# Kernel optimization log

Hardware: AMD Instinct MI355X
Metric: run time of the kernel (lower is better)

The kernel has to match this reference:

```python
import jax, jax.numpy as jnp
import numpy as np

B, C, W, H = 8192, 512, 14, 4
D = C // H  # head dim = 128


def setup_inputs() -> dict:
    key = jax.random.key(0)
    ks = jax.random.split(key, 8)
    s = 1.0 / np.sqrt(C).astype(np.float32)
    return {
        "x": jax.random.normal(ks[0], (B, C, W), jnp.float32),
        "Wq": jax.random.normal(ks[1], (C, C), jnp.float32) * s,
        "bq": jax.random.normal(ks[2], (C,), jnp.float32) * 0.01,
        "Wk": jax.random.normal(ks[3], (C, C), jnp.float32) * s,
        "bk": jax.random.normal(ks[4], (C,), jnp.float32) * 0.01,
        "Wv": jax.random.normal(ks[5], (C, C), jnp.float32) * s,
        "bv": jax.random.normal(ks[6], (C,), jnp.float32) * 0.01,
        "rel_w": jax.random.normal(ks[7], (1, H, D, W), jnp.float32),
    }


def reference(x, Wq, bq, Wk, bk, Wv, bv, rel_w):
    # Conv1d(kernel_size=1) == channel-wise linear: out[b,o,w] = sum_c Wm[o,c]*x[b,c,w] + bm[o]
    def proj(Wm, bm):
        y = jnp.einsum('oc,bcw->bow', Wm, x) + bm[None, :, None]
        return y.reshape(B, H, D, W)

    q = proj(Wq, bq)  # [B,H,D,W]
    k = proj(Wk, bk)
    v = proj(Wv, bv)

    # content-content: q^T k over head dim -> [B,H,W,W]
    cc = jnp.einsum('bhdi,bhdj->bhij', q, k)
    # content-position: rel_w^T q -> [B,H,W,W] (rows = relative position, cols = query pos)
    cp = jnp.einsum('hdi,bhdj->bhij', rel_w[0], q)

    attn = jax.nn.softmax(cc + cp, axis=-1)  # softmax over last dim, as in the original

    # out = v @ attn^T : out[b,h,d,i] = sum_j v[b,h,d,j] * attn[b,h,i,j]
    out = jnp.einsum('bhdj,bhij->bhdi', v, attn)
    return out.reshape(B, C, W)
```

## Files before the change

### kernel.cpp

```cpp
#include <hip/hip_runtime.h>
#include <hip/hip_bf16.h>

typedef __bf16 bf16x8 __attribute__((ext_vector_type(8)));
typedef float f32x4 __attribute__((ext_vector_type(4)));
typedef int i32x4 __attribute__((ext_vector_type(4)));

typedef __attribute__((address_space(1))) const void GVoid;
typedef __attribute__((address_space(3))) void LVoid;

#define SX1 16.0f
#define SX1I 0.0625f
#define SX2 4000.0f
#define SW1 400.0f
#define SW1I 0.0025f
#define SW2 100000.0f
#define SR1 32.0f
#define SR1I 0.03125f
#define SR2 8000.0f
#define SC_QK 1.5625e-4f
#define SC_CP 1.953125e-3f
#define CORR 0.004f
#define QKS 4096.0f
#define QKSI 2.44140625e-4f
#define CPS 256.0f
#define CPSI 3.90625e-3f

static __device__ __forceinline__ float b2f(unsigned short u) {
    union { float f; unsigned int i; } x; x.i = ((unsigned int)u) << 16; return x.f;
}
static __device__ __forceinline__ unsigned short f2b(float f) {
    union { float f; unsigned int u; } x; x.f = f;
    unsigned int r = x.u + 0x7FFFu + ((x.u >> 16) & 1u);
    return (unsigned short)(r >> 16);
}
static __device__ __forceinline__ int q8v(float v, float s) {
    int i = __float2int_rn(v * s);
    return (i > 127) ? 127 : (i < -127 ? -127 : i);
}
static __device__ __forceinline__ short f2s(float v, float s) {
    int i = __float2int_rn(v * s);
    i = (i > 32767) ? 32767 : (i < -32767 ? -32767 : i);
    return (short)i;
}
static __device__ __forceinline__ float s2f(unsigned int pair, int hi, float sc) {
    short s = hi ? (short)(pair >> 16) : (short)(pair & 0xffffu);
    return (float)s * sc;
}

__global__ __launch_bounds__(256) void k_prep(const float* __restrict__ Wq, const float* __restrict__ Wk,
                                              const float* __restrict__ Wv, const float* __restrict__ bq,
                                              const float* __restrict__ bk, const float* __restrict__ bv,
                                              const float* __restrict__ relw, char* __restrict__ Wi8,
                                              float* __restrict__ biasA) {
    int o = blockIdx.x;
    int tid = threadIdx.x;
    if (o < 1024) {
        const float* src = (o < 512) ? (Wq + (long)o * 512) : (Wk + (long)(o - 512) * 512);
        char* row = Wi8 + (long)o * 1024;
        for (int c = tid; c < 512; c += 256) {
            float w = src[c];
            int wh = q8v(w, SW1);
            float res = w - (float)wh * SW1I;
            int wl = q8v(res, SW2);
            row[c] = (char)wh;
            row[512 + c] = (char)wl;
        }
    } else if (o < 1536) {
        const float* src = Wv + (long)(o - 1024) * 512;
        char* row = Wi8 + (long)(1152 + (o - 1024)) * 1024;
        for (int c = tid; c < 512; c += 256) {
            float w = src[c];
            int wh = q8v(w, SW1);
            float res = w - (float)wh * SW1I;
            int wl = q8v(res, SW2);
            row[c] = (char)wh;
            row[512 + c] = (char)wl;
        }
    } else if (o < 1592) {
        int t = o - 1536, h = t / 14, i = t - h * 14;
        char* row = Wi8 + (long)(1024 + t) * 1024;
#pragma unroll
        for (int cc = 0; cc < 2; ++cc) {
            int c = tid + cc * 256;
            float acc = 0.f;
            for (int d = 0; d < 128; ++d)
                acc += relw[h * 1792 + d * 14 + i] * Wq[(long)(h * 128 + d) * 512 + c];
            int rh = q8v(acc, SR1);
            float res = acc - (float)rh * SR1I;
            int rl = q8v(res, SR2);
            row[c] = (char)rh;
            row[512 + c] = (char)rl;
        }
        if (tid == 0) {
            float acc = 0.f;
            for (int d = 0; d < 128; ++d) acc += relw[h * 1792 + d * 14 + i] * bq[h * 128 + d];
            biasA[1024 + t] = acc;
        }
    } else {
        for (int i = tid; i < 1664; i += 256) {
            if (i >= 1024 && i < 1080) continue;
            biasA[i] = (i < 512) ? bq[i] : (i < 1024) ? bk[i - 512] : (i < 1152) ? 0.f : bv[i - 1152];
        }
        int* z = (int*)(Wi8 + (long)1080 * 1024);
        for (int idx = tid; idx < 72 * 256; idx += 256) z[idx] = 0;
    }
}

__global__ __launch_bounds__(256) void k_transpose(const float* __restrict__ x,
                                                   char* __restrict__ Ai8, int b0) {
    __shared__ float xl[512 * 15];
    const float* xb = x + (long)(b0 + blockIdx.x) * 7168;
    const float4* xb4 = (const float4*)xb;
    int tid = threadIdx.x;
#pragma unroll
    for (int it = 0; it < 7; ++it) {
        int f = tid + it * 256;
        float4 v = xb4[f];
        float vals[4] = {v.x, v.y, v.z, v.w};
        int e = f * 4;
#pragma unroll
        for (int j = 0; j < 4; ++j) {
            int ee = e + j;
            int c = (ee * 9363) >> 17;
            int w = ee - c * 14;
            xl[c * 15 + w] = vals[j];
        }
    }
    __syncthreads();
    char* irow = Ai8 + (long)blockIdx.x * 14336;
#pragma unroll
    for (int it = 0; it < 7; ++it) {
        int p = tid + it * 256;
        int w = p >> 7, c0 = (p & 127) * 4;
        unsigned int hp = 0, lp = 0;
#pragma unroll
        for (int j = 0; j < 4; ++j) {
            float v = xl[(c0 + j) * 15 + w];
            int xh = q8v(v, SX1);
            float res = v - (float)xh * SX1I;
            int xlo = q8v(res, SX2);
            hp |= ((unsigned int)(xh & 255)) << (8 * j);
            lp |= ((unsigned int)(xlo & 255)) << (8 * j);
        }
        *(unsigned int*)(irow + (long)w * 1024 + c0) = hp;
        *(unsigned int*)(irow + (long)w * 1024 + 512 + c0) = lp;
    }
}

__global__ __launch_bounds__(256, 2) void k_gemmA(const char* __restrict__ Ai8,
                                                  const char* __restrict__ Wi8,
                                                  const float* __restrict__ biasA,
                                                  short* __restrict__ qkI,
                                                  unsigned short* __restrict__ vb, int Mtiles) {
    __shared__ __align__(16) char Ls[2][4][128 * 64];
    int nwg = Mtiles * 13;
    int p = blockIdx.x;
    int xcd = p & 7, o8 = p >> 3;
    int q8_ = nwg >> 3, r8 = nwg & 7;
    int t = (xcd < r8 ? xcd * (q8_ + 1) : r8 * (q8_ + 1) + (xcd - r8) * q8_) + o8;
    int mt = t / 13, nt = t - mt * 13;
    long m0 = (long)mt * 128;
    int n0 = nt * 128;
    int tid = threadIdx.x, lane = tid & 63, wv = tid >> 6;
    int wr = wv >> 1, wc = wv & 1;

    i32x4 accM[4][4], accC[4][4];
#pragma unroll
    for (int i = 0; i < 4; ++i)
#pragma unroll
        for (int j = 0; j < 4; ++j) { accM[i][j] = (i32x4){0, 0, 0, 0}; accC[i][j] = (i32x4){0, 0, 0, 0}; }

#define STAGE(KT, BUF)                                                                           \
    {                                                                                            \
        int kof = (KT) * 64;                                                                     \
        _Pragma("unroll") for (int i = 0; i < 2; ++i) {                                          \
            int row = i * 64 + (tid >> 2);                                                       \
            int gu = (((tid & 3) + (row >> 1)) & 3) << 4;                                        \
            long ao = ((m0 + row) << 10) + kof + gu;                                             \
            long bo = ((long)(n0 + row) << 10) + kof + gu;                                       \
            int dof = i * 4096 + tid * 16;                                                       \
            __builtin_amdgcn_global_load_lds((GVoid*)(Ai8 + ao), (LVoid*)(&Ls[BUF][0][0] + dof), 16, 0, 0); \
            __builtin_amdgcn_global_load_lds((GVoid*)(Ai8 + ao + 512), (LVoid*)(&Ls[BUF][1][0] + dof), 16, 0, 0); \
            __builtin_amdgcn_global_load_lds((GVoid*)(Wi8 + bo), (LVoid*)(&Ls[BUF][2][0] + dof), 16, 0, 0); \
            __builtin_amdgcn_global_load_lds((GVoid*)(Wi8 + bo + 512), (LVoid*)(&Ls[BUF][3][0] + dof), 16, 0, 0); \
        }                                                                                        \
    }

    STAGE(0, 0);
    int cur = 0;
    for (int kt = 0; kt < 8; ++kt) {
        if (kt < 7) {
            if (cur == 0) STAGE(kt + 1, 1) else STAGE(kt + 1, 0);
            asm volatile("s_waitcnt vmcnt(8)" ::: "memory");
        } else {
            asm volatile("s_waitcnt vmcnt(0)" ::: "memory");
        }
        __builtin_amdgcn_s_barrier();
        __builtin_amdgcn_sched_barrier(0);

        const char* Ah = &Ls[cur][0][0];
        const char* Al = &Ls[cur][1][0];
        const char* Bh = &Ls[cur][2][0];
        const char* Bl = &Ls[cur][3][0];
        int U = lane >> 4;
        i32x4 ah[4], al[4], bh[4], bl[4];
#pragma unroll
        for (int mf = 0; mf < 4; ++mf) {
            int row = wr * 64 + mf * 16 + (lane & 15);
            int off = row * 64 + (((U - (row >> 1)) & 3) << 4);
            ah[mf] = *(const i32x4*)(Ah + off);
            al[mf] = *(const i32x4*)(Al + off);
        }
#pragma unroll
        for (int nf = 0; nf < 4; ++nf) {
            int row = wc * 64 + nf * 16 + (lane & 15);
            int off = row * 64 + (((U - (row >> 1)) & 3) << 4);
            bh[nf] = *(const i32x4*)(Bh + off);
            bl[nf] = *(const i32x4*)(Bl + off);
        }
#pragma unroll
        for (int mf = 0; mf < 4; ++mf)
#pragma unroll
            for (int nf = 0; nf < 4; ++nf) {
                accM[mf][nf] = __builtin_amdgcn_mfma_i32_16x16x64_i8(ah[mf], bh[nf], accM[mf][nf], 0, 0, 0);
                accC[mf][nf] = __builtin_amdgcn_mfma_i32_16x16x64_i8(ah[mf], bl[nf], accC[mf][nf], 0, 0, 0);
                accC[mf][nf] = __builtin_amdgcn_mfma_i32_16x16x64_i8(al[mf], bh[nf], accC[mf][nf], 0, 0, 0);
            }
        __builtin_amdgcn_sched_barrier(0);
        __builtin_amdgcn_s_barrier();
        cur ^= 1;
    }
#undef STAGE

#pragma unroll
    for (int nf = 0; nf < 4; ++nf) {
        int n = n0 + wc * 64 + nf * 16 + (lane & 15);
        float scale = (n < 1024) ? SC_QK : (n < 1152 ? SC_CP : SC_QK);
        float bb = biasA[n];
#pragma unroll
        for (int mf = 0; mf < 4; ++mf) {
            long mg = m0 + wr * 64 + mf * 16 + ((lane >> 4) << 2);
#pragma unroll
            for (int r = 0; r < 4; ++r) {
                float val = ((float)accM[mf][nf][r] + CORR * (float)accC[mf][nf][r]) * scale + bb;
                if (n < 1024)       qkI[(mg + r) * 1152 + n] = f2s(val, QKS);
                else if (n < 1080)  qkI[(mg + r) * 1152 + n] = f2s(val, CPS);
                else if (n >= 1152) vb[(mg + r) * 512 + (n - 1152)] = f2b(val);
            }
        }
    }
}

__global__ __launch_bounds__(512) void k_attn(const short* __restrict__ qkI,
                                              const unsigned short* __restrict__ vb,
                                              float* __restrict__ out, int b0) {
    __shared__ float qs[14 * 512];
    __shared__ float ks[14 * 512];
    __shared__ float cps[56 * 16];
    __shared__ float sl[56 * 16];
    __shared__ unsigned short vs[14 * 512];
    int tid = threadIdx.x;
    long mb = (long)blockIdx.x * 14;
    const uint4* qk16 = (const uint4*)qkI;
#pragma unroll
    for (int it = 0; it < 4; ++it) {
        int idx = tid + it * 512;
        if (idx < 1792) {
            int w = idx >> 7, c8 = idx & 127;
            uint4 raw = qk16[(mb + w) * 144 + c8];
            float4 f0 = make_float4(s2f(raw.x, 0, QKSI), s2f(raw.x, 1, QKSI),
                                    s2f(raw.y, 0, QKSI), s2f(raw.y, 1, QKSI));
            float4 f1 = make_float4(s2f(raw.z, 0, QKSI), s2f(raw.z, 1, QKSI),
                                    s2f(raw.w, 0, QKSI), s2f(raw.w, 1, QKSI));
            float* base = (c8 < 64) ? qs : ks;
            int uu0 = (c8 & 63) * 2;
            *(float4*)&base[w * 512 + ((uu0 ^ (w & 7)) << 2)] = f0;
            *(float4*)&base[w * 512 + (((uu0 + 1) ^ (w & 7)) << 2)] = f1;
        }
    }
#pragma unroll
    for (int it = 0; it < 2; ++it) {
        int idx = tid + it * 512;
        if (idx < 784) {
            int w = idx / 56, tt = idx - w * 56;
            cps[tt * 16 + w] = (float)qkI[(mb + w) * 1152 + 1024 + tt] * CPSI;
        }
    }
#pragma unroll
    for (int it = 0; it < 2; ++it) {
        int idx = tid + it * 512;
        if (idx < 896) {
            int w = idx >> 6, uu = idx & 63;
            *(uint4*)&vs[w * 512 + uu * 8] = *(const uint4*)&vb[(mb + w) * 512 + uu * 8];
        }
    }
    __syncthreads();
    if (tid < 196) {
        int h = tid / 49, r = tid - h * 49;
        int i0 = (r / 7) * 2, j0 = (r - (r / 7) * 7) * 2;
        float a00 = 0.f, a01 = 0.f, a10 = 0.f, a11 = 0.f;
#pragma unroll
        for (int d4 = 0; d4 < 32; ++d4) {
            int uu = h * 32 + d4;
            float4 qa = *(const float4*)&qs[i0 * 512 + ((uu ^ (i0 & 7)) << 2)];
            float4 qb = *(const float4*)&qs[(i0 + 1) * 512 + ((uu ^ ((i0 + 1) & 7)) << 2)];
            float4 ka = *(const float4*)&ks[j0 * 512 + ((uu ^ (j0 & 7)) << 2)];
            float4 kb = *(const float4*)&ks[(j0 + 1) * 512 + ((uu ^ ((j0 + 1) & 7)) << 2)];
            a00 += qa.x * ka.x + qa.y * ka.y + qa.z * ka.z + qa.w * ka.w;
            a01 += qa.x * kb.x + qa.y * kb.y + qa.z * kb.z + qa.w * kb.w;
            a10 += qb.x * ka.x + qb.y * ka.y + qb.z * ka.z + qb.w * ka.w;
            a11 += qb.x * kb.x + qb.y * kb.y + qb.z * kb.z + qb.w * kb.w;
        }
        int base = (h * 14 + i0) * 16 + j0;
        sl[base] = a00 + cps[base];
        sl[base + 1] = a01 + cps[base + 1];
        sl[base + 16] = a10 + cps[base + 16];
        sl[base + 17] = a11 + cps[base + 17];
    }
    __syncthreads();
    if (tid < 56) {
        float* row = &sl[tid * 16];
        float m = row[0];
#pragma unroll
        for (int j = 1; j < 14; ++j) m = fmaxf(m, row[j]);
        float ex[14]; float sum = 0.f;
#pragma unroll
        for (int j = 0; j < 14; ++j) { ex[j] = __expf(row[j] - m); sum += ex[j]; }
        float inv = 1.f / sum;
#pragma unroll
        for (int j = 0; j < 14; ++j) row[j] = ex[j] * inv;
    }
    __syncthreads();
    int c = tid, h = c >> 7;
    float vr[14];
#pragma unroll
    for (int j = 0; j < 14; ++j) vr[j] = b2f(vs[j * 512 + c]);
    float* orow = out + (((long)(b0 + blockIdx.x) * 512 + c) * 14);
    float ob[14];
#pragma unroll
    for (int i = 0; i < 14; ++i) {
        const float* ar = &sl[(h * 14 + i) * 16];
        float a = 0.f;
#pragma unroll
        for (int j = 0; j < 14; ++j) a += vr[j] * ar[j];
        ob[i] = a;
    }
#pragma unroll
    for (int t2 = 0; t2 < 7; ++t2)
        *(float2*)(orow + t2 * 2) = make_float2(ob[2 * t2], ob[2 * t2 + 1]);
}

extern "C" void kernel_launch(void* const* d_in, const int* in_sizes, int n_in,
                              void* d_out, int out_size, void* d_ws, size_t ws_size,
                              hipStream_t stream) {
    const float* x    = (const float*)d_in[0];
    const float* Wq   = (const float*)d_in[1];
    const float* bq   = (const float*)d_in[2];
    const float* Wk   = (const float*)d_in[3];
    const float* bk   = (const float*)d_in[4];
    const float* Wv   = (const float*)d_in[5];
    const float* bv   = (const float*)d_in[6];
    const float* relw = (const float*)d_in[7];
    float* out = (float*)d_out;
    char* ws = (char*)d_ws;

    char*  Wi8   = ws;
    float* biasA = (float*)(ws + 1703936);
    const long WS_DATA = 1712128;

    long avail = (long)ws_size - WS_DATA;
    long nbmax = avail / 60928;
    long NBc = (nbmax / 128) * 128;
    if (NBc > 8192) NBc = 8192;
    if (NBc < 128) NBc = 128;

    char*           Ai8 = ws + WS_DATA;
    short*          qkI = (short*)(Ai8 + NBc * 14336);
    unsigned short* vbw = (unsigned short*)(qkI + NBc * 16128);

    k_prep<<<1593, 256, 0, stream>>>(Wq, Wk, Wv, bq, bk, bv, relw, Wi8, biasA);

    for (int b0 = 0; b0 < 8192; b0 += (int)NBc) {
        int nb = 8192 - b0; if (nb > NBc) nb = (int)NBc;
        int Mtiles = (nb * 14) / 128;
        k_transpose<<<nb, 256, 0, stream>>>(x, Ai8, b0);
        k_gemmA<<<Mtiles * 13, 256, 0, stream>>>(Ai8, Wi8, biasA, qkI, vbw, Mtiles);
        k_attn<<<nb, 512, 0, stream>>>(qkI, vbw, out, b0);
    }
}
```

Measured before the change: 735.2 us.

## Stage GEMM epilogue through swizzled LDS for coalesced 16-byte stores

```diff
diff --git a/kernel.cpp b/kernel.cpp
--- a/kernel.cpp
+++ b/kernel.cpp
@@ -161,6 +161,7 @@
     int mt = t / 13, nt = t - mt * 13;
     long m0 = (long)mt * 128;
     int n0 = nt * 128;
+    bool isv = (nt >= 9);
     int tid = threadIdx.x, lane = tid & 63, wv = tid >> 6;
     int wr = wv >> 1, wc = wv & 1;
 
@@ -207,46 +208,75 @@
 #pragma unroll
         for (int mf = 0; mf < 4; ++mf) {
             int row = wr * 64 + mf * 16 + (lane & 15);
-            int off = row * 64 + (((U - (row >> 1)) & 3) << 4);
-            ah[mf] = *(const i32x4*)(Ah + off);
-            al[mf] = *(const i32x4*)(Al + off);
+            ah[mf] = *(const i32x4*)(Ah + row * 64 + (((U - (row >> 1)) & 3) << 4));
         }
 #pragma unroll
         for (int nf = 0; nf < 4; ++nf) {
             int row = wc * 64 + nf * 16 + (lane & 15);
-            int off = row * 64 + (((U - (row >> 1)) & 3) << 4);
-            bh[nf] = *(const i32x4*)(Bh + off);
-            bl[nf] = *(const i32x4*)(Bl + off);
-        }
+            bh[nf] = *(const i32x4*)(Bh + row * 64 + (((U - (row >> 1)) & 3) << 4));
+        }
+#pragma unroll
+        for (int mf = 0; mf < 4; ++mf) {
+            int row = wr * 64 + mf * 16 + (lane & 15);
+            al[mf] = *(const i32x4*)(Al + row * 64 + (((U - (row >> 1)) & 3) << 4));
+        }
+#pragma unroll
+        for (int nf = 0; nf < 4; ++nf) {
+            int row = wc * 64 + nf * 16 + (lane & 15);
+            bl[nf] = *(const i32x4*)(Bl + row * 64 + (((U - (row >> 1)) & 3) << 4));
+        }
+        __builtin_amdgcn_s_setprio(1);
 #pragma unroll
         for (int mf = 0; mf < 4; ++mf)
 #pragma unroll
+            for (int nf = 0; nf < 4; ++nf)
+                accM[mf][nf] = __builtin_amdgcn_mfma_i32_16x16x64_i8(ah[mf], bh[nf], accM[mf][nf], 0, 0, 0);
+#pragma unroll
+        for (int mf = 0; mf < 4; ++mf)
+#pragma unroll
             for (int nf = 0; nf < 4; ++nf) {
-                accM[mf][nf] = __builtin_amdgcn_mfma_i32_16x16x64_i8(ah[mf], bh[nf], accM[mf][nf], 0, 0, 0);
                 accC[mf][nf] = __builtin_amdgcn_mfma_i32_16x16x64_i8(ah[mf], bl[nf], accC[mf][nf], 0, 0, 0);
                 accC[mf][nf] = __builtin_amdgcn_mfma_i32_16x16x64_i8(al[mf], bh[nf], accC[mf][nf], 0, 0, 0);
             }
+        __builtin_amdgcn_s_setprio(0);
         __builtin_amdgcn_sched_barrier(0);
         __builtin_amdgcn_s_barrier();
         cur ^= 1;
     }
 #undef STAGE
 
+    unsigned short* eb = (unsigned short*)&Ls[0][0][0];
 #pragma unroll
     for (int nf = 0; nf < 4; ++nf) {
-        int n = n0 + wc * 64 + nf * 16 + (lane & 15);
+        int ncol = wc * 64 + nf * 16 + (lane & 15);
+        int n = n0 + ncol;
         float scale = (n < 1024) ? SC_QK : (n < 1152 ? SC_CP : SC_QK);
+        float qsc = (n < 1024) ? QKS : CPS;
         float bb = biasA[n];
 #pragma unroll
         for (int mf = 0; mf < 4; ++mf) {
-            long mg = m0 + wr * 64 + mf * 16 + ((lane >> 4) << 2);
+            int rl0 = wr * 64 + mf * 16 + ((lane >> 4) << 2);
 #pragma unroll
             for (int r = 0; r < 4; ++r) {
                 float val = ((float)accM[mf][nf][r] + CORR * (float)accC[mf][nf][r]) * scale + bb;
-                if (n < 1024)       qkI[(mg + r) * 1152 + n] = f2s(val, QKS);
-                else if (n < 1080)  qkI[(mg + r) * 1152 + n] = f2s(val, CPS);
-                else if (n >= 1152) vb[(mg + r) * 512 + (n - 1152)] = f2b(val);
+                unsigned short sv = isv ? f2b(val) : (unsigned short)f2s(val, qsc);
+                int row = rl0 + r;
+                eb[row * 128 + ((((ncol >> 3) ^ (row & 7)) << 3) | (ncol & 7))] = sv;
             }
+        }
+    }
+    __syncthreads();
+    {
+        int row = tid >> 1, half = tid & 1;
+        long rb = isv ? ((m0 + row) * 1024 + (long)(n0 - 1152) * 2)
+                      : ((m0 + row) * 2304 + (long)n0 * 2);
+        char* dst = (isv ? (char*)vb : (char*)qkI) + rb + half * 128;
+        const char* src = (const char*)eb + row * 256;
+#pragma unroll
+        for (int j = 0; j < 8; ++j) {
+            int u = half * 8 + j;
+            int up = u ^ (row & 7);
+            *(uint4*)(dst + j * 16) = *(const uint4*)(src + up * 16);
         }
     }
 }
```

Measured after the change: 668.5 us. -9.1%, faster.
